# Kernel tuning notes

Measured on AMD Instinct MI355X. Metric: run time of the kernel, lower is better.

## Reference

```python
import jax, jax.numpy as jnp
import numpy as np

B, L, D = 16, 2048, 256

def setup_inputs() -> dict:
    key = jax.random.key(0)
    k1, k2 = jax.random.split(key)
    inp = jax.random.normal(k1, (B, L, D), dtype=jnp.float32)
    # Linear(2*dim, 1, bias=False) weight, torch layout [out=1, in=2*dim]
    v_w = jax.random.normal(k2, (1, 2 * D), dtype=jnp.float32) * (1.0 / np.sqrt(2 * D))
    return {"inp": inp, "v_w": v_w}


def reference(inp, v_w):
    # score[b,i,j] = cat(query=inp[b,i], key=inp[b,j]) . v_w
    # decomposes exactly into two rank-1 projections broadcast-summed.
    dim = inp.shape[-1]
    wq = v_w[0, :dim]   # multiplies the query half (unsqueeze(1) -> index i)
    wk = v_w[0, dim:]   # multiplies the key half (unsqueeze(2) -> index j)
    sq = jnp.einsum('bld,d->bl', inp, wq)          # [B,L]
    sk = jnp.einsum('bld,d->bl', inp, wk)          # [B,L]
    score = sq[:, :, None] + sk[:, None, :]        # [B,L,L]
    attn = jax.nn.softmax(score, axis=2)           # Softmax(2)
    out = jnp.einsum('bij,bjd->bid', attn, inp)    # bmm
    return (out, attn)
```

## Files before the change

### kernel.cpp

```cpp
#include <hip/hip_runtime.h>

#define BB 16
#define LL 2048
#define DD 256
#define D1B 2048
#define OUTB 256
#define D2B 2048
#define ATTB (D2B - OUTB)

typedef float vf4 __attribute__((ext_vector_type(4)));

__global__ void __launch_bounds__(256)
d1_pass(const float* __restrict__ inp, const float* __restrict__ wk,
        float* __restrict__ e, float* __restrict__ upart, float* __restrict__ zpart) {
    const int t = threadIdx.x, lane = t & 63, wid = t >> 6;
    const int blk = blockIdx.x;
    const int row0 = blk * 16 + wid * 4;

    const float4 w = *reinterpret_cast<const float4*>(wk + lane * 4);
    float4 acc = make_float4(0.f, 0.f, 0.f, 0.f);
    float zsum = 0.f;

    #pragma unroll
    for (int r = 0; r < 4; ++r) {
        const int row = row0 + r;
        const float4 a = *reinterpret_cast<const float4*>(inp + (size_t)row * DD + lane * 4);
        float dot = a.x * w.x + a.y * w.y + a.z * w.z + a.w * w.w;
        #pragma unroll
        for (int off = 32; off >= 1; off >>= 1) dot += __shfl_xor(dot, off, 64);
        const float ev = __expf(dot);
        if (lane == 0) e[row] = ev;
        zsum += ev;
        acc.x = fmaf(ev, a.x, acc.x);
        acc.y = fmaf(ev, a.y, acc.y);
        acc.z = fmaf(ev, a.z, acc.z);
        acc.w = fmaf(ev, a.w, acc.w);
    }

    __shared__ float uacc[4][DD];
    __shared__ float zw[4];
    *reinterpret_cast<float4*>(&uacc[wid][lane * 4]) = acc;
    if (lane == 0) zw[wid] = zsum;
    __syncthreads();
    upart[(size_t)blk * DD + t] = uacc[0][t] + uacc[1][t] + uacc[2][t] + uacc[3][t];
    if (t == 0) zpart[blk] = zw[0] + zw[1] + zw[2] + zw[3];
}

__global__ void __launch_bounds__(256)
d2_write(const float* __restrict__ upart, const float* __restrict__ zpart,
         const float* __restrict__ e, float* __restrict__ out) {
    const int blk = blockIdx.x, t = threadIdx.x;
    __shared__ float zs[256];
    __shared__ float invZ[BB];
    {
        int b = t >> 4, c = t & 15;
        const float* zp = zpart + b * 128 + c * 8;
        float s = 0.f;
        #pragma unroll
        for (int i = 0; i < 8; ++i) s += zp[i];
        zs[t] = s;
    }
    __syncthreads();
    if (t < BB) {
        float z = 0.f;
        #pragma unroll
        for (int c = 0; c < 16; ++c) z += zs[t * 16 + c];
        invZ[t] = 1.0f / z;
    }
    __syncthreads();

    const size_t OUT4 = (size_t)BB * LL * DD / 4;
    vf4* dst4 = (vf4*)out;

    if (blk < OUTB) {
        const int b = blk >> 4;
        const float* up = upart + ((size_t)b * 128) * DD + t;
        float acc = 0.f;
        #pragma unroll 8
        for (int c = 0; c < 128; ++c) acc += up[(size_t)c * DD];
        __shared__ float ov[DD];
        ov[t] = acc * invZ[b];
        __syncthreads();
        const vf4* ovv = (const vf4*)ov;
        vf4* dst = dst4 + (size_t)blk * 8192;
        #pragma unroll 4
        for (int it = 0; it < 32; ++it) {
            int idx = it * 256 + t;
            __builtin_nontemporal_store(ovv[idx & 63], &dst[idx]);
        }
    } else {
        const vf4* e4 = (const vf4*)e;
        const size_t ATT4 = (size_t)BB * LL * LL / 4;
        const size_t stride = (size_t)ATTB * 256;
        for (size_t k = (size_t)(blk - OUTB) * 256 + t; k < ATT4; k += stride) {
            size_t b = k >> 20, j4 = k & 511;
            vf4 v = e4[(b << 9) + j4];
            v *= invZ[b];
            __builtin_nontemporal_store(v, &dst4[OUT4 + k]);
        }
    }
}

extern "C" void kernel_launch(void* const* d_in, const int* in_sizes, int n_in,
                              void* d_out, int out_size, void* d_ws, size_t ws_size,
                              hipStream_t stream) {
    const float* inp = (const float*)d_in[0];
    const float* vw  = (const float*)d_in[1];
    float* out = (float*)d_out;
    float* ws  = (float*)d_ws;

    float* e     = ws;
    float* upart = ws + 32768;
    float* zpart = ws + 557056;

    d1_pass <<<D1B, 256, 0, stream>>>(inp, vw + DD, e, upart, zpart);
    d2_write<<<D2B, 256, 0, stream>>>(upart, zpart, e, out);
}
```

Baseline: 65.64 us.

## Fuse two passes into one kernel with per-batch atomic counters and flags

Merges the reduction pass and the write pass into one persistent-style kernel of 1024 blocks. Each block computes its partial sums and bumps a per-batch counter. One block per batch waits on that counter, reduces the partials and publishes the normalized output vector and 1/Z through a flag, and all blocks of that batch spin on the flag before streaming their slices of out and attn. This removes a kernel launch boundary and the redundant Z reduction every block used to do, at the cost of a memset launch and a deadlock risk if the 1024 blocks cannot all be resident at once.

After: 239.6 us. 3.65x slower.

```diff
diff --git a/kernel.cpp b/kernel.cpp
--- a/kernel.cpp
+++ b/kernel.cpp
@@ -3,100 +3,118 @@
 #define BB 16
 #define LL 2048
 #define DD 256
-#define D1B 2048
-#define OUTB 256
-#define D2B 2048
-#define ATTB (D2B - OUTB)
+#define NB 1024
+#define RPB 32
 
 typedef float vf4 __attribute__((ext_vector_type(4)));
 
-__global__ void __launch_bounds__(256)
-d1_pass(const float* __restrict__ inp, const float* __restrict__ wk,
-        float* __restrict__ e, float* __restrict__ upart, float* __restrict__ zpart) {
+#define OFS_E      0
+#define OFS_UPART  32768
+#define OFS_ZPART  294912
+#define OFS_OUTV   295936
+#define OFS_ZINV   300032
+#define OFS_CTR    300048
+#define OFS_FLG    300064
+
+__global__ void __launch_bounds__(256, 4)
+fused(const float* __restrict__ inp, const float* __restrict__ vw,
+      float* __restrict__ out, float* __restrict__ ws) {
     const int t = threadIdx.x, lane = t & 63, wid = t >> 6;
     const int blk = blockIdx.x;
-    const int row0 = blk * 16 + wid * 4;
+    const int b = blk >> 6;
+    const int c = blk & 63;
 
-    const float4 w = *reinterpret_cast<const float4*>(wk + lane * 4);
-    float4 acc = make_float4(0.f, 0.f, 0.f, 0.f);
-    float zsum = 0.f;
+    float* e     = ws + OFS_E;
+    float* upart = ws + OFS_UPART;
+    float* zpart = ws + OFS_ZPART;
+    float* outv  = ws + OFS_OUTV;
+    float* Zinv  = ws + OFS_ZINV;
+    int*   ctr   = (int*)(ws + OFS_CTR);
+    int*   flg   = (int*)(ws + OFS_FLG);
 
-    #pragma unroll
-    for (int r = 0; r < 4; ++r) {
-        const int row = row0 + r;
-        const float4 a = *reinterpret_cast<const float4*>(inp + (size_t)row * DD + lane * 4);
-        float dot = a.x * w.x + a.y * w.y + a.z * w.z + a.w * w.w;
+    {
+        const float4 w = *reinterpret_cast<const float4*>(vw + DD + lane * 4);
+        float4 acc = make_float4(0.f, 0.f, 0.f, 0.f);
+        float zsum = 0.f;
+        const int row0 = blk * RPB + wid * 8;
         #pragma unroll
-        for (int off = 32; off >= 1; off >>= 1) dot += __shfl_xor(dot, off, 64);
-        const float ev = __expf(dot);
-        if (lane == 0) e[row] = ev;
-        zsum += ev;
-        acc.x = fmaf(ev, a.x, acc.x);
-        acc.y = fmaf(ev, a.y, acc.y);
-        acc.z = fmaf(ev, a.z, acc.z);
-        acc.w = fmaf(ev, a.w, acc.w);
+        for (int r = 0; r < 8; ++r) {
+            const int row = row0 + r;
+            const float4 a = *reinterpret_cast<const float4*>(inp + (size_t)row * DD + lane * 4);
+            float dot = a.x * w.x + a.y * w.y + a.z * w.z + a.w * w.w;
+            #pragma unroll
+            for (int off = 32; off >= 1; off >>= 1) dot += __shfl_xor(dot, off, 64);
+            const float ev = __expf(dot);
+            if (lane == 0) e[row] = ev;
+            zsum += ev;
+            acc.x = fmaf(ev, a.x, acc.x);
+            acc.y = fmaf(ev, a.y, acc.y);
+            acc.z = fmaf(ev, a.z, acc.z);
+            acc.w = fmaf(ev, a.w, acc.w);
+        }
+        __shared__ float uacc[4][DD];
+        __shared__ float zw[4];
+        *reinterpret_cast<float4*>(&uacc[wid][lane * 4]) = acc;
+        if (lane == 0) zw[wid] = zsum;
+        __syncthreads();
+        upart[(size_t)blk * DD + t] = uacc[0][t] + uacc[1][t] + uacc[2][t] + uacc[3][t];
+        if (t == 0) zpart[blk] = zw[0] + zw[1] + zw[2] + zw[3];
+        __syncthreads();
+        if (t == 0) {
+            __threadfence();
+            __hip_atomic_fetch_add(&ctr[b], 1, __ATOMIC_RELEASE, __HIP_MEMORY_SCOPE_AGENT);
+        }
     }
 
-    __shared__ float uacc[4][DD];
-    __shared__ float zw[4];
-    *reinterpret_cast<float4*>(&uacc[wid][lane * 4]) = acc;
-    if (lane == 0) zw[wid] = zsum;
-    __syncthreads();
-    upart[(size_t)blk * DD + t] = uacc[0][t] + uacc[1][t] + uacc[2][t] + uacc[3][t];
-    if (t == 0) zpart[blk] = zw[0] + zw[1] + zw[2] + zw[3];
-}
-
-__global__ void __launch_bounds__(256)
-d2_write(const float* __restrict__ upart, const float* __restrict__ zpart,
-         const float* __restrict__ e, float* __restrict__ out) {
-    const int blk = blockIdx.x, t = threadIdx.x;
-    __shared__ float zs[256];
-    __shared__ float invZ[BB];
-    {
-        int b = t >> 4, c = t & 15;
-        const float* zp = zpart + b * 128 + c * 8;
-        float s = 0.f;
-        #pragma unroll
-        for (int i = 0; i < 8; ++i) s += zp[i];
-        zs[t] = s;
-    }
-    __syncthreads();
-    if (t < BB) {
-        float z = 0.f;
-        #pragma unroll
-        for (int c = 0; c < 16; ++c) z += zs[t * 16 + c];
-        invZ[t] = 1.0f / z;
-    }
-    __syncthreads();
-
-    const size_t OUT4 = (size_t)BB * LL * DD / 4;
-    vf4* dst4 = (vf4*)out;
-
-    if (blk < OUTB) {
-        const int b = blk >> 4;
-        const float* up = upart + ((size_t)b * 128) * DD + t;
+    if (c == 0) {
+        if (t == 0) {
+            while (__hip_atomic_load(&ctr[b], __ATOMIC_ACQUIRE, __HIP_MEMORY_SCOPE_AGENT) < 64)
+                __builtin_amdgcn_s_sleep(8);
+        }
+        __syncthreads();
+        __shared__ float sInv;
+        if (wid == 0) {
+            float z = zpart[b * 64 + lane];
+            #pragma unroll
+            for (int off = 32; off >= 1; off >>= 1) z += __shfl_xor(z, off, 64);
+            if (lane == 0) sInv = 1.0f / z;
+        }
+        __syncthreads();
+        const float iz = sInv;
         float acc = 0.f;
         #pragma unroll 8
-        for (int c = 0; c < 128; ++c) acc += up[(size_t)c * DD];
-        __shared__ float ov[DD];
-        ov[t] = acc * invZ[b];
+        for (int k = 0; k < 64; ++k) acc += upart[(size_t)(b * 64 + k) * DD + t];
+        outv[b * DD + t] = acc * iz;
+        if (t == 0) Zinv[b] = iz;
         __syncthreads();
-        const vf4* ovv = (const vf4*)ov;
-        vf4* dst = dst4 + (size_t)blk * 8192;
+        if (t == 0) {
+            __threadfence();
+            __hip_atomic_store(&flg[b], 1, __ATOMIC_RELEASE, __HIP_MEMORY_SCOPE_AGENT);
+        }
+    }
+
+    {
+        while (__hip_atomic_load(&flg[b], __ATOMIC_ACQUIRE, __HIP_MEMORY_SCOPE_AGENT) == 0)
+            __builtin_amdgcn_s_sleep(2);
+
+        const float iz = Zinv[b];
+        const vf4* e4 = (const vf4*)e;
+        vf4 ev0 = e4[(b << 9) + t] * iz;
+        vf4 ev1 = e4[(b << 9) + 256 + t] * iz;
+
+        vf4* dst = (vf4*)out;
+        const vf4* ov4 = (const vf4*)outv;
+        vf4 ov = ov4[(b << 6) + (t & 63)];
+        size_t obase = (size_t)b * 131072 + (size_t)c * 2048 + t;
+        #pragma unroll
+        for (int it = 0; it < 8; ++it)
+            __builtin_nontemporal_store(ov, &dst[obase + (size_t)it * 256]);
+
+        size_t abase = (size_t)2097152 + (size_t)b * 1048576 + (size_t)c * 16384 + t;
         #pragma unroll 4
-        for (int it = 0; it < 32; ++it) {
-            int idx = it * 256 + t;
-            __builtin_nontemporal_store(ovv[idx & 63], &dst[idx]);
-        }
-    } else {
-        const vf4* e4 = (const vf4*)e;
-        const size_t ATT4 = (size_t)BB * LL * LL / 4;
-        const size_t stride = (size_t)ATTB * 256;
-        for (size_t k = (size_t)(blk - OUTB) * 256 + t; k < ATT4; k += stride) {
-            size_t b = k >> 20, j4 = k & 511;
-            vf4 v = e4[(b << 9) + j4];
-            v *= invZ[b];
-            __builtin_nontemporal_store(v, &dst4[OUT4 + k]);
+        for (int it = 0; it < 64; it += 2) {
+            __builtin_nontemporal_store(ev0, &dst[abase + (size_t)it * 256]);
+            __builtin_nontemporal_store(ev1, &dst[abase + (size_t)it * 256 + 256]);
         }
     }
 }
@@ -109,10 +127,6 @@
     float* out = (float*)d_out;
     float* ws  = (float*)d_ws;
 
-    float* e     = ws;
-    float* upart = ws + 32768;
-    float* zpart = ws + 557056;
-
-    d1_pass <<<D1B, 256, 0, stream>>>(inp, vw + DD, e, upart, zpart);
-    d2_write<<<D2B, 256, 0, stream>>>(upart, zpart, e, out);
+    hipMemsetAsync((char*)d_ws + (size_t)OFS_CTR * 4, 0, 128, stream);
+    fused<<<NB, 256, 0, stream>>>(inp, vw, out, ws);
 }
```

## Assign one batch per write block, hoist attn row loads, use plain stores

Applied to the files above, without the earlier changes.

The write kernel now gives each block a fixed batch. Each block reduces only that batch's partition sums with a wave shuffle instead of summing all 16 batches through shared memory. Attention blocks load their row's exp values once into registers and store them repeatedly, replacing the strided grid loop with per-iteration index math and loads. The grid grows to 2304 blocks, and nontemporal stores become ordinary stores, which may change cache write behaviour for the 256MB output.

Result: slower. 71.29 us (+8.6%).

```diff
diff --git a/kernel.cpp b/kernel.cpp
--- a/kernel.cpp
+++ b/kernel.cpp
@@ -5,8 +5,7 @@
 #define DD 256
 #define D1B 2048
 #define OUTB 256
-#define D2B 2048
-#define ATTB (D2B - OUTB)
+#define ATTB 2048
 
 typedef float vf4 __attribute__((ext_vector_type(4)));
 
@@ -50,53 +49,46 @@
 d2_write(const float* __restrict__ upart, const float* __restrict__ zpart,
          const float* __restrict__ e, float* __restrict__ out) {
     const int blk = blockIdx.x, t = threadIdx.x;
-    __shared__ float zs[256];
-    __shared__ float invZ[BB];
-    {
-        int b = t >> 4, c = t & 15;
-        const float* zp = zpart + b * 128 + c * 8;
-        float s = 0.f;
+    const int lane = t & 63, wid = t >> 6;
+    __shared__ float sInv;
+    __shared__ float ov[DD];
+
+    const bool isOut = blk < OUTB;
+    const int b = isOut ? (blk >> 4) : ((blk - OUTB) >> 7);
+
+    if (wid == 0) {
+        const float2 z2 = *reinterpret_cast<const float2*>(zpart + b * 128 + lane * 2);
+        float z = z2.x + z2.y;
         #pragma unroll
-        for (int i = 0; i < 8; ++i) s += zp[i];
-        zs[t] = s;
+        for (int off = 32; off >= 1; off >>= 1) z += __shfl_xor(z, off, 64);
+        if (lane == 0) sInv = 1.0f / z;
     }
     __syncthreads();
-    if (t < BB) {
-        float z = 0.f;
-        #pragma unroll
-        for (int c = 0; c < 16; ++c) z += zs[t * 16 + c];
-        invZ[t] = 1.0f / z;
-    }
-    __syncthreads();
+    const float iz = sInv;
+    vf4* dst = (vf4*)out;
 
-    const size_t OUT4 = (size_t)BB * LL * DD / 4;
-    vf4* dst4 = (vf4*)out;
-
-    if (blk < OUTB) {
-        const int b = blk >> 4;
+    if (isOut) {
         const float* up = upart + ((size_t)b * 128) * DD + t;
         float acc = 0.f;
         #pragma unroll 8
-        for (int c = 0; c < 128; ++c) acc += up[(size_t)c * DD];
-        __shared__ float ov[DD];
-        ov[t] = acc * invZ[b];
+        for (int k = 0; k < 128; ++k) acc += up[(size_t)k * DD];
+        ov[t] = acc * iz;
         __syncthreads();
-        const vf4* ovv = (const vf4*)ov;
-        vf4* dst = dst4 + (size_t)blk * 8192;
+        const vf4 o = ((const vf4*)ov)[t & 63];
+        size_t obase = (size_t)b * 131072 + (size_t)(blk & 15) * 8192 + t;
         #pragma unroll 4
-        for (int it = 0; it < 32; ++it) {
-            int idx = it * 256 + t;
-            __builtin_nontemporal_store(ovv[idx & 63], &dst[idx]);
-        }
+        for (int it = 0; it < 32; ++it)
+            dst[obase + (size_t)it * 256] = o;
     } else {
+        const int s = (blk - OUTB) & 127;
         const vf4* e4 = (const vf4*)e;
-        const size_t ATT4 = (size_t)BB * LL * LL / 4;
-        const size_t stride = (size_t)ATTB * 256;
-        for (size_t k = (size_t)(blk - OUTB) * 256 + t; k < ATT4; k += stride) {
-            size_t b = k >> 20, j4 = k & 511;
-            vf4 v = e4[(b << 9) + j4];
-            v *= invZ[b];
-            __builtin_nontemporal_store(v, &dst4[OUT4 + k]);
+        const vf4 ev0 = e4[(b << 9) + t] * iz;
+        const vf4 ev1 = e4[(b << 9) + 256 + t] * iz;
+        size_t abase = (size_t)2097152 + (size_t)b * 1048576 + (size_t)s * 8192 + t;
+        #pragma unroll 4
+        for (int it = 0; it < 32; it += 2) {
+            dst[abase + (size_t)it * 256]       = ev0;
+            dst[abase + (size_t)it * 256 + 256] = ev1;
         }
     }
 }
@@ -114,5 +106,5 @@
     float* zpart = ws + 557056;
 
     d1_pass <<<D1B, 256, 0, stream>>>(inp, vw + DD, e, upart, zpart);
-    d2_write<<<D2B, 256, 0, stream>>>(upart, zpart, e, out);
+    d2_write<<<OUTB + ATTB, 256, 0, stream>>>(upart, zpart, e, out);
 }
```
